# Kernel tuning notes

Hardware: AMD Instinct MI355X
Metric: run time of the kernel (lower is better)

Reference implementation:

```python
import jax, jax.numpy as jnp
import numpy as np

B, SEQ, DIM = 32, 512, 1024
DEPTH, HEADS, DHEAD = 6, 8, 64
INNER = HEADS * DHEAD  # 512
NLAT, MAXSEQ = 64, 512
EPS = 1e-5


def setup_inputs() -> dict:
    key = jax.random.key(0)
    ks = jax.random.split(key, 8)
    return {
        "x": jax.random.normal(ks[0], (B, SEQ, DIM), dtype=jnp.float32),
        "attention_mask": jax.random.randint(ks[1], (B, SEQ), 0, 2, dtype=jnp.int32),
        "latents": jax.random.normal(ks[2], (NLAT, DIM), dtype=jnp.float32),
        "media_pos_emb": jax.random.normal(ks[3], (MAXSEQ, DIM), dtype=jnp.float32),
        "ln_media_g": jnp.ones((DEPTH, DIM), jnp.float32),
        "ln_media_b": jnp.zeros((DEPTH, DIM), jnp.float32),
        "ln_lat_g": jnp.ones((DEPTH, DIM), jnp.float32),
        "ln_lat_b": jnp.zeros((DEPTH, DIM), jnp.float32),
        "Wq": jax.random.normal(ks[4], (DEPTH, DIM, INNER), dtype=jnp.float32) * 0.02,
        "Wkv": jax.random.normal(ks[5], (DEPTH, DIM, 2 * INNER), dtype=jnp.float32) * 0.02,
        "Wout": jax.random.normal(ks[6], (DEPTH, INNER, DIM), dtype=jnp.float32) * 0.02,
        "final_g": jnp.ones((DIM,), jnp.float32),
        "final_b": jnp.zeros((DIM,), jnp.float32),
    }


def _layer_norm(x, g, b):
    mu = jnp.mean(x, axis=-1, keepdims=True)
    var = jnp.mean(jnp.square(x - mu), axis=-1, keepdims=True)
    return (x - mu) * jax.lax.rsqrt(var + EPS) * g + b


def _heads(t):
    # b n (h d) -> b h n d
    b, n, _ = t.shape
    return t.reshape(b, n, HEADS, DHEAD).transpose(0, 2, 1, 3)


def reference(x, attention_mask, latents, media_pos_emb, ln_media_g, ln_media_b,
              ln_lat_g, ln_lat_b, Wq, Wkv, Wout, final_g, final_b):
    b, seq, _ = x.shape
    x = x + media_pos_emb[None, :seq, :]
    lat = jnp.broadcast_to(latents[None], (b, NLAT, DIM))
    scale = DHEAD ** -0.5
    # key mask over [latents ++ media]: latent keys never masked; 1 == masked
    key_mask = jnp.concatenate(
        [jnp.zeros((b, NLAT), attention_mask.dtype), attention_mask], axis=1)
    masked = (key_mask == 1)[:, None, None, :]  # b 1 1 j
    for l in range(DEPTH):
        xm = _layer_norm(x, ln_media_g[l], ln_media_b[l])
        ln = _layer_norm(lat, ln_lat_g[l], ln_lat_b[l])
        q = _heads(ln @ Wq[l])                      # b h i d
        kv = jnp.concatenate([ln, xm], axis=1) @ Wkv[l]
        k, v = jnp.split(kv, 2, axis=-1)
        k, v = _heads(k), _heads(v)                 # b h j d
        sim = jnp.einsum('bhid,bhjd->bhij', q * scale, k)
        sim = jnp.where(masked, -jnp.inf, sim)
        attn = jax.nn.softmax(sim, axis=-1)
        out = jnp.einsum('bhij,bhjd->bhid', attn, v)
        out = out.transpose(0, 2, 1, 3).reshape(b, NLAT, INNER)
        lat = lat + out @ Wout[l]
    return _layer_norm(lat, final_g, final_b)
```

## Files before the change

kernel.cpp:

```cpp
#include <hip/hip_runtime.h>
#include <cstdint>


#define DEVINL __device__ __forceinline__

typedef __attribute__((ext_vector_type(8))) short short8_t;
typedef __attribute__((ext_vector_type(4))) float f32x4;

DEVINL ushort f2bf(float f) {
  union { float f; uint32_t u; } c; c.f = f;
  uint32_t u = c.u;
  u += ((u >> 16) & 1u) + 0x7fffu;
  return (ushort)(u >> 16);
}
DEVINL float bf2f(ushort u) {
  union { uint32_t u; float f; } c; c.u = ((uint32_t)u) << 16;
  return c.f;
}
DEVINL f32x4 mfma16(short8_t a, short8_t b, f32x4 c) {
  return __builtin_amdgcn_mfma_f32_16x16x32_bf16(a, b, c, 0, 0, 0);
}
DEVINL void gld16(ushort* lds, const ushort* g) {
  __builtin_amdgcn_global_load_lds(
      (const __attribute__((address_space(1))) void*)g,
      (__attribute__((address_space(3))) void*)lds, 16, 0, 0);
}

__global__ __launch_bounds__(512, 2) void k_gemm256m(const ushort* __restrict__ A,
    const ushort* __restrict__ Bt, const float* __restrict__ bias,
    ushort* __restrict__ Kb, ushort* __restrict__ Vt) {
  extern __shared__ char lds[];
  constexpr int K = 1024, NT = 16;
  int tid = threadIdx.x, lane = tid & 63, w = tid >> 6;
  int wm = w >> 2, wn = w & 3;
  int fr = lane & 15;
  int fkb = (lane >> 4) << 4;
  int xorv = (fr & 7) << 4;
  int bid = blockIdx.x;
  int xcd = bid & 7, ii = bid >> 3;
  int m0 = (xcd * 8 + (ii >> 2)) * 256;
  int n0 = (ii & 3) * 256;
  int srow = w * 8 + (lane >> 3);
  int sce = ((lane & 7) ^ (lane >> 3)) << 3;
  const ushort* Ag = A + (size_t)(m0 + srow) * K + sce;
  const ushort* Bg = Bt + (size_t)(n0 + srow) * K + sce;
  f32x4 acc[8][4] = {};

  auto stA = [&](int t, int h) {
    ushort* d = (ushort*)(lds + (t % 3) * 32768 + h * 16384 + w * 1024);
    const ushort* s = Ag + (size_t)(h * 128) * K + t * 64;
    gld16(d, s);
    gld16((ushort*)((char*)d + 8192), s + (size_t)64 * K);
  };
  auto stB = [&](int t, int h) {
    ushort* d = (ushort*)(lds + 98304 + (t & 1) * 32768 + h * 16384 + w * 1024);
    const ushort* s = Bg + (size_t)(h * 128) * K + t * 64;
    gld16(d, s);
    gld16((ushort*)((char*)d + 8192), s + (size_t)64 * K);
  };
  stA(0, 0); stA(0, 1); stB(0, 0); stB(0, 1); stA(1, 0); stA(1, 1);

#define RD_AFR(DST, MQ)                                                        \
  _Pragma("unroll") for (int m2 = 0; m2 < 2; ++m2)                             \
    _Pragma("unroll") for (int kh = 0; kh < 2; ++kh)                           \
      DST[m2][kh] = *(const short8_t*)(ab +                                    \
          ((wm * 128 + (MQ + m2) * 16 + fr) << 7) + ((kh * 64 + fkb) ^ xorv));

#define CLUSTER(MQ, AFR)                                                       \
  __builtin_amdgcn_s_setprio(1);                                               \
  _Pragma("unroll") for (int kh = 0; kh < 2; ++kh)                             \
    _Pragma("unroll") for (int m2 = 0; m2 < 2; ++m2)                           \
      _Pragma("unroll") for (int nt = 0; nt < 4; ++nt)                         \
        acc[MQ + m2][nt] = mfma16(AFR[m2][kh], bfr[nt][kh], acc[MQ + m2][nt]); \
  __builtin_amdgcn_s_setprio(0);                                               \
  __builtin_amdgcn_s_barrier();

  for (int t = 0; t < NT; ++t) {
    const char* ab = lds + (t % 3) * 32768;
    const char* bb = lds + 98304 + (t & 1) * 32768;
    short8_t bfr[4][2], afrX[2][2], afrY[2][2];
    if (t + 1 < NT) asm volatile("s_waitcnt vmcnt(4)" ::: "memory");
    else            asm volatile("s_waitcnt vmcnt(0)" ::: "memory");
    __builtin_amdgcn_s_barrier();
#pragma unroll
    for (int nt = 0; nt < 4; ++nt)
#pragma unroll
      for (int kh = 0; kh < 2; ++kh)
        bfr[nt][kh] = *(const short8_t*)(bb +
            ((wn * 64 + nt * 16 + fr) << 7) + ((kh * 64 + fkb) ^ xorv));
    RD_AFR(afrX, 0);
    if (t + 1 < NT) stB(t + 1, 0);
    RD_AFR(afrY, 2);
    CLUSTER(0, afrX);
    if (t + 1 < NT) stB(t + 1, 1);
    RD_AFR(afrX, 4);
    CLUSTER(2, afrY);
    if (t + 2 < NT) stA(t + 2, 0);
    RD_AFR(afrY, 6);
    CLUSTER(4, afrX);
    if (t + 2 < NT) stA(t + 2, 1);
    CLUSTER(6, afrY);
  }
#undef RD_AFR
#undef CLUSTER

  __syncthreads();
  ushort* Cl = (ushort*)lds;
  constexpr int CLS = 264;
  bool isV = (n0 >= 512);
#pragma unroll
  for (int mt = 0; mt < 8; ++mt)
#pragma unroll
    for (int nt = 0; nt < 4; ++nt)
#pragma unroll
      for (int r = 0; r < 4; ++r) {
        int rl = wm * 128 + mt * 16 + ((lane >> 4) << 2) + r;
        int cl = wn * 64 + nt * 16 + fr;
        ushort v = f2bf(acc[mt][nt][r] + bias[n0 + cl]);
        if (!isV) Cl[rl * CLS + cl] = v;
        else      Cl[cl * CLS + rl] = v;
      }
  __syncthreads();
  int b_ = m0 >> 9;
  int jb = 64 + (m0 & 511);
#pragma unroll
  for (int q2 = 0; q2 < 16; ++q2) {
    int task = tid + q2 * 512;
    int rr2 = task >> 5, c8 = task & 31;
    short8_t vv = *(const short8_t*)&Cl[rr2 * CLS + c8 * 8];
    if (!isV)
      *(short8_t*)&Kb[((size_t)(b_ * 576 + jb + rr2) << 9) + n0 + c8 * 8] = vv;
    else
      *(short8_t*)&Vt[(size_t)(b_ * 512 + (n0 - 512) + rr2) * 576 + jb + c8 * 8] = vv;
  }
}

__global__ __launch_bounds__(512) void k_attn(const ushort* __restrict__ Q,
    const ushort* __restrict__ Kb, const ushort* __restrict__ Vt,
    const int* __restrict__ amask, ushort* __restrict__ AO) {
  extern __shared__ char alds[];
  ushort* sim = (ushort*)alds;
  char* stg = alds + 74752;
  int bh = blockIdx.x;
  int h = bh & 7, b = bh >> 3;
  int tid = threadIdx.x, lane = tid & 63, w = tid >> 6;
  int rg = w >> 1, ch = w & 1;
  int fr = lane & 15;
  int fkb = (lane >> 4) << 4;
  int csrc8 = ((lane & 7) ^ (lane >> 3)) << 3;
  short8_t aq0, aq1;
  {
    int qi = rg * 16 + fr;
    const ushort* qp = Q + ((size_t)(b * 64 + qi) << 9) + h * 64 + ((lane >> 4) << 3);
    aq0 = *(const short8_t*)qp;
    aq1 = *(const short8_t*)(qp + 32);
  }
  unsigned mbits = 0;
#pragma unroll
  for (int c = 1; c < 9; ++c)
    if (amask[b * 512 + (c - 1) * 64 + lane]) mbits |= (1u << c);

  auto stageK = [&](int it, int buf) {
#pragma unroll
    for (int g = 0; g < 3; ++g) {
      int sr = w * 24 + g * 8 + (lane >> 3);
      ushort* d = (ushort*)(stg + buf * 24576 + (w * 24 + g * 8) * 128);
      gld16(d, Kb + ((size_t)(b * 576 + it * 192 + sr) << 9) + h * 64 + csrc8);
    }
  };
  auto stageV = [&](int it, int buf) {
#pragma unroll
    for (int g = 0; g < 3; ++g) {
      int sr = w * 8 + (lane >> 3);
      ushort* d = (ushort*)(stg + buf * 24576 + g * 8192 + w * 8 * 128);
      gld16(d, Vt + (size_t)(b * 512 + h * 64 + sr) * 576 + it * 192 + g * 64 + csrc8);
    }
  };

  stageK(0, 0);
  for (int it = 0; it < 3; ++it) {
    int buf = it & 1;
    __builtin_amdgcn_s_barrier();
    if (it + 1 < 3) {
      stageK(it + 1, buf ^ 1);
      asm volatile("s_waitcnt vmcnt(3)" ::: "memory");
    } else {
      asm volatile("s_waitcnt vmcnt(0)" ::: "memory");
    }
    __builtin_amdgcn_s_barrier();
    const char* kb_ = stg + buf * 24576;
#pragma unroll
    for (int ct = 0; ct < 6; ++ct) {
      int row_l = ch * 96 + ct * 16 + fr;
      const char* base = kb_ + row_l * 128;
      int sw = (row_l & 7) << 4;
      short8_t k0 = *(const short8_t*)(base + (fkb ^ sw));
      short8_t k1 = *(const short8_t*)(base + ((64 + fkb) ^ sw));
      f32x4 s4 = {};
      s4 = mfma16(aq0, k0, s4);
      s4 = mfma16(aq1, k1, s4);
#pragma unroll
      for (int r = 0; r < 4; ++r)
        sim[(rg * 16 + ((lane >> 4) << 2) + r) * 584 +
            it * 192 + ch * 96 + ct * 16 + fr] = f2bf(s4[r]);
    }
  }
  __syncthreads();
  stageV(0, 0);
  for (int rr = 0; rr < 8; ++rr) {
    int row = w * 8 + rr;
    float vals[9];
    float m = -3.0e38f;
#pragma unroll
    for (int c = 0; c < 9; ++c) {
      float v = bf2f(sim[row * 584 + c * 64 + lane]);
      vals[c] = v;
      if (!((mbits >> c) & 1)) m = fmaxf(m, v);
    }
#pragma unroll
    for (int off = 32; off; off >>= 1) m = fmaxf(m, __shfl_xor(m, off));
    float ssum = 0.f;
    float p[9];
#pragma unroll
    for (int c = 0; c < 9; ++c) {
      p[c] = ((mbits >> c) & 1) ? 0.f : __expf(vals[c] - m);
      ssum += p[c];
    }
#pragma unroll
    for (int off = 32; off; off >>= 1) ssum += __shfl_xor(ssum, off);
    float inv = 1.0f / ssum;
#pragma unroll
    for (int c = 0; c < 9; ++c)
      sim[row * 584 + c * 64 + lane] = f2bf(p[c] * inv);
  }
  __syncthreads();
  f32x4 oacc[2] = {};
  for (int it = 0; it < 3; ++it) {
    int buf = it & 1;
    __builtin_amdgcn_s_barrier();
    if (it + 1 < 3) {
      stageV(it + 1, buf ^ 1);
      asm volatile("s_waitcnt vmcnt(3)" ::: "memory");
    } else {
      asm volatile("s_waitcnt vmcnt(0)" ::: "memory");
    }
    __builtin_amdgcn_s_barrier();
#pragma unroll
    for (int g = 0; g < 3; ++g) {
      const char* vb_ = stg + buf * 24576 + g * 8192;
      const ushort* srow_ = &sim[(rg * 16 + fr) * 584 + it * 192 + g * 64];
      short8_t pa0 = *(const short8_t*)(srow_ + ((lane >> 4) << 3));
      short8_t pa1 = *(const short8_t*)(srow_ + 32 + ((lane >> 4) << 3));
#pragma unroll
      for (int dt = 0; dt < 2; ++dt) {
        int row_l = ch * 32 + dt * 16 + fr;
        const char* base = vb_ + row_l * 128;
        int sw = (row_l & 7) << 4;
        short8_t v0 = *(const short8_t*)(base + (fkb ^ sw));
        short8_t v1 = *(const short8_t*)(base + ((64 + fkb) ^ sw));
        oacc[dt] = mfma16(pa0, v0, oacc[dt]);
        oacc[dt] = mfma16(pa1, v1, oacc[dt]);
      }
    }
  }
#pragma unroll
  for (int dt = 0; dt < 2; ++dt)
#pragma unroll
    for (int r = 0; r < 4; ++r) {
      int i = rg * 16 + ((lane >> 4) << 2) + r;
      int d = ch * 32 + dt * 16 + fr;
      AO[((size_t)(b * 64 + i) << 9) + h * 64 + d] = f2bf(oacc[dt][r]);
    }
}

__global__ __launch_bounds__(256) void k_fold_kv(const float* __restrict__ Wkv,
    const float* __restrict__ lnmg, const float* __restrict__ lnlg,
    const float* __restrict__ lnmb, const float* __restrict__ lnlb,
    ushort* __restrict__ wkvmT, ushort* __restrict__ wlatT,
    float* __restrict__ pb) {
  __shared__ float tile[32][33];
  __shared__ float pm[8][32], pl[8][32];
  int l = blockIdx.z, rt = blockIdx.y;
  int c0 = blockIdx.x * 32, r0 = rt * 32;
  const float* Wl = Wkv + (size_t)l * 1048576;
  int tx = threadIdx.x & 31, ty = threadIdx.x >> 5;
#pragma unroll
  for (int i = 0; i < 4; ++i)
    tile[ty + i * 8][tx] = Wl[(size_t)(r0 + ty + i * 8) * 1024 + c0 + tx];
  __syncthreads();
  float am = 0.f, al = 0.f;
#pragma unroll
  for (int i = 0; i < 4; ++i) {
    int r = ty * 4 + i;
    float wv = tile[r][tx];
    am += lnmb[l * 1024 + r0 + r] * wv;
    al += lnlb[l * 1024 + r0 + r] * wv;
  }
  pm[ty][tx] = am; pl[ty][tx] = al;
#pragma unroll
  for (int i = 0; i < 4; ++i) {
    int c = ty + i * 8;
    float wv = tile[tx][c];
    int r = r0 + tx;
    wkvmT[(size_t)l * 1048576 + (size_t)(c0 + c) * 1024 + r] =
        f2bf(wv * lnmg[l * 1024 + r]);
    wlatT[(size_t)l * 1572864 + (size_t)(512 + c0 + c) * 1024 + r] =
        f2bf(wv * lnlg[l * 1024 + r]);
  }
  __syncthreads();
  if (ty == 0) {
    float sm = 0.f, sl = 0.f;
#pragma unroll
    for (int k = 0; k < 8; ++k) { sm += pm[k][tx]; sl += pl[k][tx]; }
    pb[(size_t)(l * 32 + rt) * 2560 + c0 + tx] = sm;
    pb[(size_t)(l * 32 + rt) * 2560 + 1536 + c0 + tx] = sl;
  }
}

__global__ __launch_bounds__(256) void k_fold_q(const float* __restrict__ Wq,
    const float* __restrict__ lnlg, const float* __restrict__ lnlb,
    ushort* __restrict__ wlatT, float* __restrict__ pb) {
  __shared__ float tile[32][33];
  __shared__ float pq[8][32];
  int l = blockIdx.z, rt = blockIdx.y;
  int c0 = blockIdx.x * 32, r0 = rt * 32;
  const float* Wl = Wq + (size_t)l * 524288;
  int tx = threadIdx.x & 31, ty = threadIdx.x >> 5;
#pragma unroll
  for (int i = 0; i < 4; ++i)
    tile[ty + i * 8][tx] = Wl[(size_t)(r0 + ty + i * 8) * 512 + c0 + tx];
  __syncthreads();
  float aq = 0.f;
#pragma unroll
  for (int i = 0; i < 4; ++i) {
    int r = ty * 4 + i;
    aq += lnlb[l * 1024 + r0 + r] * tile[r][tx];
  }
  pq[ty][tx] = aq;
#pragma unroll
  for (int i = 0; i < 4; ++i) {
    int c = ty + i * 8;
    float wv = tile[tx][c];
    int r = r0 + tx;
    wlatT[(size_t)l * 1572864 + (size_t)(c0 + c) * 1024 + r] =
        f2bf(wv * lnlg[l * 1024 + r] * 0.125f);
  }
  __syncthreads();
  if (ty == 0) {
    float s = 0.f;
#pragma unroll
    for (int k = 0; k < 8; ++k) s += pq[k][tx];
    pb[(size_t)(l * 32 + rt) * 2560 + 1024 + c0 + tx] = s;
  }
}

__global__ __launch_bounds__(256) void k_bias_red(const float* __restrict__ pb,
    float* __restrict__ bkvm, float* __restrict__ blat) {
  int l = blockIdx.y;
  int c = blockIdx.x * 256 + threadIdx.x;
  float s = 0.f;
  for (int rt = 0; rt < 32; ++rt)
    s += pb[(size_t)(l * 32 + rt) * 2560 + c];
  if (c < 1024)       bkvm[l * 1024 + c] = s;
  else if (c < 1536)  blat[l * 1536 + (c - 1024)] = s * 0.125f;
  else                blat[l * 1536 + 512 + (c - 1536)] = s;
}

__global__ __launch_bounds__(256) void k_fold_out(const float* __restrict__ Wout,
    ushort* __restrict__ woutT) {
  __shared__ float tile[32][33];
  int l = blockIdx.z;
  const float* Wl = Wout + (size_t)l * 524288;
  int r0 = blockIdx.y * 32, c0 = blockIdx.x * 32;
  int tx = threadIdx.x & 31, ty = threadIdx.x >> 5;
#pragma unroll
  for (int i = 0; i < 4; ++i)
    tile[ty + i * 8][tx] = Wl[(size_t)(r0 + ty + i * 8) * 1024 + c0 + tx];
  __syncthreads();
#pragma unroll
  for (int i = 0; i < 4; ++i) {
    int jl = ty + i * 8;
    woutT[(size_t)l * 524288 + (size_t)(c0 + jl) * 512 + r0 + tx] = f2bf(tile[tx][jl]);
  }
}

__global__ __launch_bounds__(256) void k_rownorm(const float* __restrict__ in,
    const float* __restrict__ pos, ushort* __restrict__ out) {
  int row = blockIdx.x, t = threadIdx.x;
  float4 v = *(const float4*)(in + (size_t)row * 1024 + t * 4);
  if (pos) {
    float4 p = *(const float4*)(pos + (size_t)(row & 511) * 1024 + t * 4);
    v.x += p.x; v.y += p.y; v.z += p.z; v.w += p.w;
  }
  float s = v.x + v.y + v.z + v.w;
  float q = v.x * v.x + v.y * v.y + v.z * v.z + v.w * v.w;
#pragma unroll
  for (int off = 32; off; off >>= 1) { s += __shfl_xor(s, off); q += __shfl_xor(q, off); }
  __shared__ float rs[4], rq[4];
  if ((t & 63) == 0) { rs[t >> 6] = s; rq[t >> 6] = q; }
  __syncthreads();
  s = rs[0] + rs[1] + rs[2] + rs[3];
  q = rq[0] + rq[1] + rq[2] + rq[3];
  float mean = s * (1.0f / 1024.0f);
  float var = q * (1.0f / 1024.0f) - mean * mean;
  float rstd = rsqrtf(var + 1e-5f);
  ushort4 o;
  o.x = f2bf((v.x - mean) * rstd);
  o.y = f2bf((v.y - mean) * rstd);
  o.z = f2bf((v.z - mean) * rstd);
  o.w = f2bf((v.w - mean) * rstd);
  *(ushort4*)(out + (size_t)row * 1024 + t * 4) = o;
}

__global__ __launch_bounds__(256) void k_finalln(const float* __restrict__ in,
    const float* __restrict__ g, const float* __restrict__ b, float* __restrict__ out) {
  int row = blockIdx.x, t = threadIdx.x;
  float4 v = *(const float4*)(in + (size_t)row * 1024 + t * 4);
  float s = v.x + v.y + v.z + v.w;
  float q = v.x * v.x + v.y * v.y + v.z * v.z + v.w * v.w;
#pragma unroll
  for (int off = 32; off; off >>= 1) { s += __shfl_xor(s, off); q += __shfl_xor(q, off); }
  __shared__ float rs[4], rq[4];
  if ((t & 63) == 0) { rs[t >> 6] = s; rq[t >> 6] = q; }
  __syncthreads();
  s = rs[0] + rs[1] + rs[2] + rs[3];
  q = rq[0] + rq[1] + rq[2] + rq[3];
  float mean = s * (1.0f / 1024.0f);
  float var = q * (1.0f / 1024.0f) - mean * mean;
  float rstd = rsqrtf(var + 1e-5f);
  float4 g4 = *(const float4*)(g + t * 4);
  float4 b4 = *(const float4*)(b + t * 4);
  float4 o;
  o.x = (v.x - mean) * rstd * g4.x + b4.x;
  o.y = (v.y - mean) * rstd * g4.y + b4.y;
  o.z = (v.z - mean) * rstd * g4.z + b4.z;
  o.w = (v.w - mean) * rstd * g4.w + b4.w;
  *(float4*)(out + (size_t)row * 1024 + t * 4) = o;
}

__global__ __launch_bounds__(256) void k_latinit(const float* __restrict__ latents,
                                                 float* __restrict__ lat) {
  int row = blockIdx.x, t = threadIdx.x;
  *(float4*)(lat + (size_t)row * 1024 + t * 4) =
      *(const float4*)(latents + (size_t)(row & 63) * 1024 + t * 4);
}

template <int MODE>
__global__ __launch_bounds__(256) void k_gemm64(const ushort* __restrict__ A,
    const ushort* __restrict__ Bt, const float* __restrict__ bias,
    ushort* __restrict__ o0, ushort* __restrict__ o1, ushort* __restrict__ o2,
    float* __restrict__ of, int N, int K) {
  __shared__ ushort Al[2][64][32];
  __shared__ ushort Bl[2][64][32];
  __shared__ ushort Cl[64][72];
  int tid = threadIdx.x, lane = tid & 63, w = tid >> 6;
  int wr = w >> 1, wc = w & 1;
  int m0 = blockIdx.y * 64, n0 = blockIdx.x * 64;
  f32x4 acc[2][2] = {};
  const ushort* Ag = A + (size_t)(m0 + w * 16 + (lane >> 2)) * K + (lane & 3) * 8;
  const ushort* Bg = Bt + (size_t)(n0 + w * 16 + (lane >> 2)) * K + (lane & 3) * 8;
  int fr = lane & 15, fk = (lane >> 4) << 3;
  int nt = K >> 5;
  gld16(&Al[0][w * 16][0], Ag);
  gld16(&Bl[0][w * 16][0], Bg);
  for (int t = 0; t < nt; ++t) {
    int cur = t & 1;
    if (t + 1 < nt) {
      int k0 = (t + 1) << 5;
      gld16(&Al[cur ^ 1][w * 16][0], Ag + k0);
      gld16(&Bl[cur ^ 1][w * 16][0], Bg + k0);
      asm volatile("s_waitcnt vmcnt(2)" ::: "memory");
    } else {
      asm volatile("s_waitcnt vmcnt(0)" ::: "memory");
    }
    __builtin_amdgcn_s_barrier();
    short8_t a[2], b[2];
#pragma unroll
    for (int mt = 0; mt < 2; ++mt)
      a[mt] = *(const short8_t*)&Al[cur][wr * 32 + mt * 16 + fr][fk];
#pragma unroll
    for (int nt2 = 0; nt2 < 2; ++nt2)
      b[nt2] = *(const short8_t*)&Bl[cur][wc * 32 + nt2 * 16 + fr][fk];
#pragma unroll
    for (int mt = 0; mt < 2; ++mt)
#pragma unroll
      for (int nt2 = 0; nt2 < 2; ++nt2)
        acc[mt][nt2] = mfma16(a[mt], b[nt2], acc[mt][nt2]);
    __builtin_amdgcn_s_barrier();
  }
  if constexpr (MODE == 3) {
    if (n0 >= 1024) {
#pragma unroll
      for (int mt = 0; mt < 2; ++mt)
#pragma unroll
        for (int nt2 = 0; nt2 < 2; ++nt2)
#pragma unroll
          for (int r = 0; r < 4; ++r) {
            int rl = wr * 32 + mt * 16 + ((lane >> 4) << 2) + r;
            int col = wc * 32 + nt2 * 16 + (lane & 15);
            Cl[rl][col] = f2bf(acc[mt][nt2][r] + bias[n0 + col]);
          }
      __syncthreads();
      int b_ = m0 >> 6;
#pragma unroll
      for (int q = 0; q < 2; ++q) {
        int task = tid + q * 256;
        int jg = task & 7, d = task >> 3;
        short8_t vv;
#pragma unroll
        for (int e = 0; e < 8; ++e) vv[e] = (short)Cl[jg * 8 + e][d];
        *(short8_t*)&o2[((size_t)(b_ * 512 + (n0 - 1024) + d)) * 576 + jg * 8] = vv;
      }
      return;
    }
  }
#pragma unroll
  for (int mt = 0; mt < 2; ++mt)
#pragma unroll
    for (int nt2 = 0; nt2 < 2; ++nt2)
#pragma unroll
      for (int r = 0; r < 4; ++r) {
        int row = m0 + wr * 32 + mt * 16 + ((lane >> 4) << 2) + r;
        int col = n0 + wc * 32 + nt2 * 16 + (lane & 15);
        float v = acc[mt][nt2][r] + (bias ? bias[col] : 0.0f);
        if constexpr (MODE == 3) {
          int b_ = row >> 6, ii = row & 63;
          if (col < 512) o0[(size_t)row * 512 + col] = f2bf(v);
          else           o1[(((size_t)(b_ * 576 + ii)) << 9) + (col - 512)] = f2bf(v);
        } else {
          of[(size_t)row * N + col] += v;
        }
      }
}

extern "C" void kernel_launch(void* const* d_in, const int* in_sizes, int n_in,
                              void* d_out, int out_size, void* d_ws, size_t ws_size,
                              hipStream_t stream) {
  const float* x       = (const float*)d_in[0];
  const int*   amask   = (const int*)d_in[1];
  const float* latents = (const float*)d_in[2];
  const float* pos     = (const float*)d_in[3];
  const float* lnmg    = (const float*)d_in[4];
  const float* lnmb    = (const float*)d_in[5];
  const float* lnlg    = (const float*)d_in[6];
  const float* lnlb    = (const float*)d_in[7];
  const float* Wq      = (const float*)d_in[8];
  const float* Wkv     = (const float*)d_in[9];
  const float* Wout    = (const float*)d_in[10];
  const float* fg      = (const float*)d_in[11];
  const float* fb      = (const float*)d_in[12];
  float* out = (float*)d_out;
  char* ws = (char*)d_ws;

  ushort* xhat  = (ushort*)(ws + 0);
  ushort* wkvmT = (ushort*)(ws + 33554432);
  ushort* wlatT = (ushort*)(ws + 46137344);
  ushort* woutT = (ushort*)(ws + 65011712);
  float*  bkvm  = (float*)(ws + 71303168);
  float*  blat  = (float*)(ws + 71327744);
  float*  lat   = (float*)(ws + 71364608);
  ushort* lhat  = (ushort*)(ws + 79753216);
  ushort* qbuf  = (ushort*)(ws + 83947520);
  ushort* Kbuf  = (ushort*)(ws + 86044672);
  ushort* Vt    = (ushort*)(ws + 104919040);
  ushort* aobuf = (ushort*)(ws + 123793408);
  float*  pb    = (float*)(ws + 125890560);

  (void)hipFuncSetAttribute((const void*)k_gemm256m,
                            hipFuncAttributeMaxDynamicSharedMemorySize, 163840);
  (void)hipFuncSetAttribute((const void*)k_attn,
                            hipFuncAttributeMaxDynamicSharedMemorySize, 131072);

  dim3 B256(256);
  k_fold_kv<<<dim3(32, 32, 6), B256, 0, stream>>>(Wkv, lnmg, lnlg, lnmb, lnlb,
                                                  wkvmT, wlatT, pb);
  k_fold_q<<<dim3(16, 32, 6), B256, 0, stream>>>(Wq, lnlg, lnlb, wlatT, pb);
  k_fold_out<<<dim3(32, 16, 6), B256, 0, stream>>>(Wout, woutT);
  k_bias_red<<<dim3(10, 6), B256, 0, stream>>>(pb, bkvm, blat);
  k_rownorm<<<16384, B256, 0, stream>>>(x, pos, xhat);
  k_latinit<<<2048, B256, 0, stream>>>(latents, lat);

  for (int l = 0; l < 6; ++l) {
    k_rownorm<<<2048, B256, 0, stream>>>(lat, nullptr, lhat);
    k_gemm64<3><<<dim3(24, 32), B256, 0, stream>>>(
        lhat, wlatT + (size_t)l * 1572864, blat + l * 1536,
        qbuf, Kbuf, Vt, nullptr, 1536, 1024);
    k_gemm256m<<<dim3(256), dim3(512), 163840, stream>>>(
        xhat, wkvmT + (size_t)l * 1048576, bkvm + l * 1024, Kbuf, Vt);
    k_attn<<<dim3(256), dim3(512), 123904, stream>>>(qbuf, Kbuf, Vt, amask, aobuf);
    k_gemm64<2><<<dim3(16, 32), B256, 0, stream>>>(
        aobuf, woutT + (size_t)l * 524288, nullptr,
        nullptr, nullptr, nullptr, lat, 1024, 512);
  }
  k_finalln<<<2048, B256, 0, stream>>>(lat, fg, fb, out);
}
```

Before: 599.3 us.

## Shrink media KV GEMM tile from 256x256 to 128x128 with 4-wave blocks

The media K/V projection GEMM moves from 256x256 tiles with 512-thread blocks (256 blocks) to 128x128 tiles with 256-thread blocks (1024 blocks), with LDS per block halved. The interleaved cluster schedule, where A-fragment loads and MFMA groups alternated with barriers, is replaced by one load-all-then-MFMA phase per k-step. The aim is more blocks per CU and better load balance across the 256 CUs, at the cost of lower arithmetic intensity per block, more global and L2 traffic, and less overlap of LDS reads with MFMA.

```diff
diff --git a/kernel.cpp b/kernel.cpp
--- a/kernel.cpp
+++ b/kernel.cpp
@@ -26,96 +26,86 @@
       (__attribute__((address_space(3))) void*)lds, 16, 0, 0);
 }
 
-__global__ __launch_bounds__(512, 2) void k_gemm256m(const ushort* __restrict__ A,
+__global__ __launch_bounds__(256, 2) void k_gemm128m(const ushort* __restrict__ A,
     const ushort* __restrict__ Bt, const float* __restrict__ bias,
     ushort* __restrict__ Kb, ushort* __restrict__ Vt) {
   extern __shared__ char lds[];
   constexpr int K = 1024, NT = 16;
   int tid = threadIdx.x, lane = tid & 63, w = tid >> 6;
-  int wm = w >> 2, wn = w & 3;
+  int wr = w >> 1, wc = w & 1;
   int fr = lane & 15;
   int fkb = (lane >> 4) << 4;
   int xorv = (fr & 7) << 4;
   int bid = blockIdx.x;
   int xcd = bid & 7, ii = bid >> 3;
-  int m0 = (xcd * 8 + (ii >> 2)) * 256;
-  int n0 = (ii & 3) * 256;
-  int srow = w * 8 + (lane >> 3);
+  int m0 = (xcd * 16 + (ii >> 3)) * 128;
+  int n0 = (ii & 7) * 128;
   int sce = ((lane & 7) ^ (lane >> 3)) << 3;
-  const ushort* Ag = A + (size_t)(m0 + srow) * K + sce;
-  const ushort* Bg = Bt + (size_t)(n0 + srow) * K + sce;
-  f32x4 acc[8][4] = {};
-
-  auto stA = [&](int t, int h) {
-    ushort* d = (ushort*)(lds + (t % 3) * 32768 + h * 16384 + w * 1024);
-    const ushort* s = Ag + (size_t)(h * 128) * K + t * 64;
-    gld16(d, s);
-    gld16((ushort*)((char*)d + 8192), s + (size_t)64 * K);
+  const ushort* Ag = A + (size_t)(m0 + w * 32 + (lane >> 3)) * K + sce;
+  const ushort* Bg = Bt + (size_t)(n0 + w * 32 + (lane >> 3)) * K + sce;
+  f32x4 acc[4][4] = {};
+
+  auto stA = [&](int t) {
+    char* d = lds + (t % 3) * 16384 + w * 4096;
+    const ushort* s = Ag + t * 64;
+#pragma unroll
+    for (int g = 0; g < 4; ++g)
+      gld16((ushort*)(d + g * 1024), s + (size_t)(g * 8) * K);
   };
-  auto stB = [&](int t, int h) {
-    ushort* d = (ushort*)(lds + 98304 + (t & 1) * 32768 + h * 16384 + w * 1024);
-    const ushort* s = Bg + (size_t)(h * 128) * K + t * 64;
-    gld16(d, s);
-    gld16((ushort*)((char*)d + 8192), s + (size_t)64 * K);
+  auto stB = [&](int t) {
+    char* d = lds + 49152 + (t & 1) * 16384 + w * 4096;
+    const ushort* s = Bg + t * 64;
+#pragma unroll
+    for (int g = 0; g < 4; ++g)
+      gld16((ushort*)(d + g * 1024), s + (size_t)(g * 8) * K);
   };
-  stA(0, 0); stA(0, 1); stB(0, 0); stB(0, 1); stA(1, 0); stA(1, 1);
-
-#define RD_AFR(DST, MQ)                                                        \
-  _Pragma("unroll") for (int m2 = 0; m2 < 2; ++m2)                             \
-    _Pragma("unroll") for (int kh = 0; kh < 2; ++kh)                           \
-      DST[m2][kh] = *(const short8_t*)(ab +                                    \
-          ((wm * 128 + (MQ + m2) * 16 + fr) << 7) + ((kh * 64 + fkb) ^ xorv));
-
-#define CLUSTER(MQ, AFR)                                                       \
-  __builtin_amdgcn_s_setprio(1);                                               \
-  _Pragma("unroll") for (int kh = 0; kh < 2; ++kh)                             \
-    _Pragma("unroll") for (int m2 = 0; m2 < 2; ++m2)                           \
-      _Pragma("unroll") for (int nt = 0; nt < 4; ++nt)                         \
-        acc[MQ + m2][nt] = mfma16(AFR[m2][kh], bfr[nt][kh], acc[MQ + m2][nt]); \
-  __builtin_amdgcn_s_setprio(0);                                               \
-  __builtin_amdgcn_s_barrier();
+  stA(0); stB(0); stA(1);
 
   for (int t = 0; t < NT; ++t) {
-    const char* ab = lds + (t % 3) * 32768;
-    const char* bb = lds + 98304 + (t & 1) * 32768;
-    short8_t bfr[4][2], afrX[2][2], afrY[2][2];
+    const char* ab = lds + (t % 3) * 16384;
+    const char* bb = lds + 49152 + (t & 1) * 16384;
     if (t + 1 < NT) asm volatile("s_waitcnt vmcnt(4)" ::: "memory");
     else            asm volatile("s_waitcnt vmcnt(0)" ::: "memory");
     __builtin_amdgcn_s_barrier();
+    short8_t a[4][2], b[4][2];
+#pragma unroll
+    for (int mt = 0; mt < 4; ++mt)
+#pragma unroll
+      for (int kh = 0; kh < 2; ++kh)
+        a[mt][kh] = *(const short8_t*)(ab +
+            ((wr * 64 + mt * 16 + fr) << 7) + ((kh * 64 + fkb) ^ xorv));
 #pragma unroll
     for (int nt = 0; nt < 4; ++nt)
 #pragma unroll
       for (int kh = 0; kh < 2; ++kh)
-        bfr[nt][kh] = *(const short8_t*)(bb +
-            ((wn * 64 + nt * 16 + fr) << 7) + ((kh * 64 + fkb) ^ xorv));
-    RD_AFR(afrX, 0);
-    if (t + 1 < NT) stB(t + 1, 0);
-    RD_AFR(afrY, 2);
-    CLUSTER(0, afrX);
-    if (t + 1 < NT) stB(t + 1, 1);
-    RD_AFR(afrX, 4);
-    CLUSTER(2, afrY);
-    if (t + 2 < NT) stA(t + 2, 0);
-    RD_AFR(afrY, 6);
-    CLUSTER(4, afrX);
-    if (t + 2 < NT) stA(t + 2, 1);
-    CLUSTER(6, afrY);
-  }
-#undef RD_AFR
-#undef CLUSTER
+        b[nt][kh] = *(const short8_t*)(bb +
+            ((wc * 64 + nt * 16 + fr) << 7) + ((kh * 64 + fkb) ^ xorv));
+    if (t + 1 < NT) stB(t + 1);
+    if (t + 2 < NT) stA(t + 2);
+    __builtin_amdgcn_s_setprio(1);
+#pragma unroll
+    for (int kh = 0; kh < 2; ++kh)
+#pragma unroll
+      for (int mt = 0; mt < 4; ++mt)
+#pragma unroll
+        for (int nt = 0; nt < 4; ++nt)
+          acc[mt][nt] = mfma16(a[mt][kh], b[nt][kh], acc[mt][nt]);
+    __builtin_amdgcn_s_setprio(0);
+    __builtin_amdgcn_s_barrier();
+  }
 
   __syncthreads();
   ushort* Cl = (ushort*)lds;
-  constexpr int CLS = 264;
+  constexpr int CLS = 136;
   bool isV = (n0 >= 512);
 #pragma unroll
-  for (int mt = 0; mt < 8; ++mt)
+  for (int mt = 0; mt < 4; ++mt)
 #pragma unroll
     for (int nt = 0; nt < 4; ++nt)
 #pragma unroll
       for (int r = 0; r < 4; ++r) {
-        int rl = wm * 128 + mt * 16 + ((lane >> 4) << 2) + r;
-        int cl = wn * 64 + nt * 16 + fr;
+        int rl = wr * 64 + mt * 16 + ((lane >> 4) << 2) + r;
+        int cl = wc * 64 + nt * 16 + fr;
         ushort v = f2bf(acc[mt][nt][r] + bias[n0 + cl]);
         if (!isV) Cl[rl * CLS + cl] = v;
         else      Cl[cl * CLS + rl] = v;
@@ -124,9 +114,9 @@
   int b_ = m0 >> 9;
   int jb = 64 + (m0 & 511);
 #pragma unroll
-  for (int q2 = 0; q2 < 16; ++q2) {
-    int task = tid + q2 * 512;
-    int rr2 = task >> 5, c8 = task & 31;
+  for (int q2 = 0; q2 < 8; ++q2) {
+    int task = tid + q2 * 256;
+    int rr2 = task >> 4, c8 = task & 15;
     short8_t vv = *(const short8_t*)&Cl[rr2 * CLS + c8 * 8];
     if (!isV)
       *(short8_t*)&Kb[((size_t)(b_ * 576 + jb + rr2) << 9) + n0 + c8 * 8] = vv;
@@ -566,8 +556,8 @@
   ushort* aobuf = (ushort*)(ws + 123793408);
   float*  pb    = (float*)(ws + 125890560);
 
-  (void)hipFuncSetAttribute((const void*)k_gemm256m,
-                            hipFuncAttributeMaxDynamicSharedMemorySize, 163840);
+  (void)hipFuncSetAttribute((const void*)k_gemm128m,
+                            hipFuncAttributeMaxDynamicSharedMemorySize, 81920);
   (void)hipFuncSetAttribute((const void*)k_attn,
                             hipFuncAttributeMaxDynamicSharedMemorySize, 131072);
 
@@ -585,7 +575,7 @@
     k_gemm64<3><<<dim3(24, 32), B256, 0, stream>>>(
         lhat, wlatT + (size_t)l * 1572864, blat + l * 1536,
         qbuf, Kbuf, Vt, nullptr, 1536, 1024);
-    k_gemm256m<<<dim3(256), dim3(512), 163840, stream>>>(
+    k_gemm128m<<<dim3(1024), B256, 81920, stream>>>(
         xhat, wkvmT + (size_t)l * 1048576, bkvm + l * 1024, Kbuf, Vt);
     k_attn<<<dim3(256), dim3(512), 123904, stream>>>(qbuf, Kbuf, Vt, amask, aobuf);
     k_gemm64<2><<<dim3(16, 32), B256, 0, stream>>>(
```

New measurement: 635.9 us. 6.1% more time.
